# Optimization experiments

Hardware: AMD Instinct MI355X
Metric: run time of the kernel (lower is better)

The kernel has to match this reference:

```python
import jax, jax.numpy as jnp
import numpy as np

POS_W = 1.0
ANG_W = 1.0
WID_W = 1.0
N = 1048560  # predictions (divisible by 17)
M = 8388480  # total GT grasps = sum(arange(N) % 17)


def setup_inputs() -> dict:
    key = jax.random.key(0)
    k1, k2 = jax.random.split(key)
    pred = jax.random.normal(k1, (N, 6), dtype=jnp.float32)
    all_targets = jax.random.normal(k2, (M, 6), dtype=jnp.float32)
    # ragged counts in [0, 16]; sum == M exactly
    target_counts = (jnp.arange(N, dtype=jnp.int64) % 17)
    return {"pred": pred, "all_targets": all_targets, "target_counts": target_counts}


def _smooth_l1(x):
    a = jnp.abs(x)
    return jnp.where(a < 1.0, 0.5 * x * x, a - 0.5)


def reference(pred, all_targets, target_counts):
    n = pred.shape[0]
    m = all_targets.shape[0]
    # segment id for each GT row (contiguous slices, order of target_counts)
    seg = jnp.repeat(jnp.arange(n), target_counts, total_repeat_length=m)  # (M,)
    p = pred[seg]  # (M,6) gathered predictions
    dp = p[:, :2] - all_targets[:, :2]
    da = p[:, 2:4] - all_targets[:, 2:4]
    dw = p[:, 4] - all_targets[:, 4]
    dist = (POS_W * jnp.sum(dp * dp, axis=-1)
            + ANG_W * jnp.sum(da * da, axis=-1)
            + WID_W * dw * dw)  # (M,)
    # ragged argmin per segment (first occurrence, like torch.argmin)
    min_d = jax.ops.segment_min(dist, seg, num_segments=n)  # (N,)
    row = jnp.arange(m)
    cand = jnp.where(dist == min_d[seg], row, m)
    arg = jax.ops.segment_min(cand, seg, num_segments=n)  # (N,) global row idx or m
    has = target_counts > 0
    gt = all_targets[jnp.where(has, jnp.clip(arg, 0, m - 1), 0)]  # (N,6)
    # fused per-prediction loss against the closest GT
    loss_pos = jnp.sum(_smooth_l1(pred[:, :2] - gt[:, :2]), axis=-1)
    loss_ang = jnp.sum(jnp.abs(pred[:, 2:4] - gt[:, 2:4]), axis=-1)
    loss_wid = _smooth_l1(pred[:, 4] - gt[:, 4])
    losses = jnp.where(has, POS_W * loss_pos + ANG_W * loss_ang + WID_W * loss_wid, 0.0)
    return jnp.mean(losses)  # reduction='mean'
```

## Files before the change

kernel.cpp:

```cpp
#include <hip/hip_runtime.h>
#include <math.h>
#include <stdint.h>

#define POS_W 1.0f
#define ANG_W 1.0f
#define WID_W 1.0f
#define CHUNKR 2176
#define SEGMAX 52

__device__ __forceinline__ float smooth_l1(float x) {
    float a = fabsf(x);
    return a < 1.0f ? 0.5f * x * x : a - 0.5f;
}

__device__ __forceinline__ void gl_lds16(const float4* g, float4* l) {
    __builtin_amdgcn_global_load_lds(
        (const __attribute__((address_space(1))) void*)g,
        (__attribute__((address_space(3))) void*)l, 16, 0, 0);
}

__global__ void k_block_sums(const int* __restrict__ counts, int stride, int n,
                             int* __restrict__ blockSums) {
    int i = blockIdx.x * 256 + threadIdx.x;
    int c = (i < n) ? counts[(long long)i * stride] : 0;
    for (int off = 32; off > 0; off >>= 1) c += __shfl_down(c, off, 64);
    __shared__ int sdata[4];
    int lane = threadIdx.x & 63, wave = threadIdx.x >> 6;
    if (lane == 0) sdata[wave] = c;
    __syncthreads();
    if (threadIdx.x == 0)
        blockSums[blockIdx.x] = sdata[0] + sdata[1] + sdata[2] + sdata[3];
}

__global__ __launch_bounds__(256) void k_loss(
    const float* __restrict__ pred, const float* __restrict__ tgt,
    const int* __restrict__ counts, int stride, int n, int mrows,
    const int* __restrict__ blockSums, float invN, float* __restrict__ out) {
    __shared__ float4 buf[SEGMAX * 64];
    __shared__ int wsum[4];
    __shared__ int wpre[4];
    __shared__ float fs[4];

    int t = threadIdx.x;
    int lane = t & 63, wave = t >> 6;
    int b = blockIdx.x;
    int i = b * 256 + t;
    int c = (i < n) ? counts[(long long)i * stride] : 0;

    int pre = 0;
    for (int j = t; j < b; j += 256) pre += blockSums[j];

    int incl = c;
#pragma unroll
    for (int d = 1; d < 64; d <<= 1) {
        int v = __shfl_up(incl, d, 64);
        if (lane >= d) incl += v;
    }
    for (int o = 32; o > 0; o >>= 1) pre += __shfl_down(pre, o, 64);
    if (lane == 63) wsum[wave] = incl;
    if (lane == 0) wpre[wave] = pre;

    bool active = (i < n) && (c > 0);
    float p0 = 0, p1 = 0, p2 = 0, p3 = 0, p4 = 0;
    if (active) {
        const float2* p2p = (const float2*)(pred + (long long)i * 6);
        float2 a = p2p[0], bb = p2p[1], w = p2p[2];
        p0 = a.x; p1 = a.y; p2 = bb.x; p3 = bb.y; p4 = w.x;
    }
    __syncthreads();

    int w0 = wsum[0], w1 = wsum[1], w2 = wsum[2], w3 = wsum[3];
    int waveOff = (wave > 0 ? w0 : 0) + (wave > 1 ? w1 : 0) + (wave > 2 ? w2 : 0);
    int off = waveOff + incl - c;
    int total = w0 + w1 + w2 + w3;
    int winStart = wpre[0] + wpre[1] + wpre[2] + wpre[3];

    long long winB = (long long)winStart * 24;
    long long base4 = (winB & ~15ll) >> 4;
    int sh = (int)(winStart & 1);
    long long f4last = (((long long)mrows * 24) >> 4) - 1;
    const float4* tgt4 = (const float4*)tgt;
    const float2* ch2 = (const float2*)buf;

    float best = INFINITY;
    float b0 = 0, b1 = 0, b2 = 0, b3 = 0, b4 = 0;

    for (int base = 0; base < total; base += CHUNKR) {
        int rows = min(CHUNKR, total - base);
        int nF4 = (rows * 3 + sh + 1) >> 1;
        int nSeg = (nF4 + 63) >> 6;
        long long q0 = base4 + (((long long)base * 3) >> 1);
        for (int seg = wave; seg < nSeg; seg += 4) {
            long long gi = q0 + (long long)(seg << 6) + lane;
            if (gi > f4last) gi = f4last;
            gl_lds16(tgt4 + gi, &buf[seg * 64]);
        }
        asm volatile("s_waitcnt vmcnt(0)" ::: "memory");
        __builtin_amdgcn_s_barrier();
        __builtin_amdgcn_sched_barrier(0);

        if (active) {
            int lo = max(off, base), hi = min(off + c, base + rows);
            for (int rr = lo; rr < hi; ++rr) {
                int l2i = (rr - base) * 3 + sh;
                float2 ga = ch2[l2i], gb = ch2[l2i + 1], gw = ch2[l2i + 2];
                float d0 = p0 - ga.x, d1 = p1 - ga.y;
                float d2 = p2 - gb.x, d3 = p3 - gb.y;
                float d4 = p4 - gw.x;
                float dist = POS_W * (d0 * d0 + d1 * d1) +
                             ANG_W * (d2 * d2 + d3 * d3) + WID_W * d4 * d4;
                if (dist < best) {
                    best = dist;
                    b0 = ga.x; b1 = ga.y; b2 = gb.x; b3 = gb.y; b4 = gw.x;
                }
            }
        }
        if (base + CHUNKR < total) {
            asm volatile("s_waitcnt lgkmcnt(0)" ::: "memory");
            __builtin_amdgcn_s_barrier();
            __builtin_amdgcn_sched_barrier(0);
        }
    }

    float loss = 0.0f;
    if (active) {
        loss = POS_W * (smooth_l1(p0 - b0) + smooth_l1(p1 - b1)) +
               ANG_W * (fabsf(p2 - b2) + fabsf(p3 - b3)) +
               WID_W * smooth_l1(p4 - b4);
    }

    for (int o = 32; o > 0; o >>= 1) loss += __shfl_down(loss, o, 64);
    if (lane == 0) fs[wave] = loss;
    __syncthreads();
    if (t == 0) {
        float tot = (fs[0] + fs[1] + fs[2] + fs[3]) * invN;
        atomicAdd(out, tot);
    }
}

extern "C" void kernel_launch(void* const* d_in, const int* in_sizes, int n_in,
                              void* d_out, int out_size, void* d_ws,
                              size_t ws_size, hipStream_t stream) {
    const float* pred = (const float*)d_in[0];
    const float* tgt = (const float*)d_in[1];
    const int* counts = (const int*)d_in[2];
    int n = in_sizes[0] / 6;
    int mrows = in_sizes[1] / 6;
    int stride = (in_sizes[2] == n) ? 1 : 2;
    int nb = (n + 255) / 256;

    int* blockSums = (int*)d_ws;
    float* out = (float*)d_out;

    hipMemsetAsync(d_out, 0, sizeof(float), stream);
    k_block_sums<<<nb, 256, 0, stream>>>(counts, stride, n, blockSums);
    k_loss<<<nb, 256, 0, stream>>>(pred, tgt, counts, stride, n, mrows,
                                   blockSums, 1.0f / n, out);
}
```

Before: 303.0 us.

## Split target staging into two LDS halves and compute first half early

```diff
diff --git a/kernel.cpp b/kernel.cpp
--- a/kernel.cpp
+++ b/kernel.cpp
@@ -5,8 +5,11 @@
 #define POS_W 1.0f
 #define ANG_W 1.0f
 #define WID_W 1.0f
-#define CHUNKR 2176
-#define SEGMAX 52
+#define SEGS_A 28
+#define SEGS_B 24
+#define SEGS_T (SEGS_A + SEGS_B)
+#define ROWS_A 1194
+#define ROWS_PASS 2112
 
 __device__ __forceinline__ float smooth_l1(float x) {
     float a = fabsf(x);
@@ -36,7 +39,7 @@
     const float* __restrict__ pred, const float* __restrict__ tgt,
     const int* __restrict__ counts, int stride, int n, int mrows,
     const int* __restrict__ blockSums, float invN, float* __restrict__ out) {
-    __shared__ float4 buf[SEGMAX * 64];
+    __shared__ float4 buf[SEGS_T * 64];
     __shared__ int wsum[4];
     __shared__ int wpre[4];
     __shared__ float fs[4];
@@ -47,8 +50,17 @@
     int i = b * 256 + t;
     int c = (i < n) ? counts[(long long)i * stride] : 0;
 
-    int pre = 0;
-    for (int j = t; j < b; j += 256) pre += blockSums[j];
+    int pre;
+    {
+        int s0 = 0, s1 = 0, s2 = 0, s3 = 0;
+        int j = t;
+        for (; j + 768 < b; j += 1024) {
+            s0 += blockSums[j];       s1 += blockSums[j + 256];
+            s2 += blockSums[j + 512]; s3 += blockSums[j + 768];
+        }
+        for (; j < b; j += 256) s0 += blockSums[j];
+        pre = (s0 + s1) + (s2 + s3);
+    }
 
     int incl = c;
 #pragma unroll
@@ -85,40 +97,71 @@
     float best = INFINITY;
     float b0 = 0, b1 = 0, b2 = 0, b3 = 0, b4 = 0;
 
-    for (int base = 0; base < total; base += CHUNKR) {
-        int rows = min(CHUNKR, total - base);
-        int nF4 = (rows * 3 + sh + 1) >> 1;
-        int nSeg = (nF4 + 63) >> 6;
-        long long q0 = base4 + (((long long)base * 3) >> 1);
-        for (int seg = wave; seg < nSeg; seg += 4) {
-            long long gi = q0 + (long long)(seg << 6) + lane;
-            if (gi > f4last) gi = f4last;
-            gl_lds16(tgt4 + gi, &buf[seg * 64]);
-        }
-        asm volatile("s_waitcnt vmcnt(0)" ::: "memory");
-        __builtin_amdgcn_s_barrier();
-        __builtin_amdgcn_sched_barrier(0);
-
-        if (active) {
-            int lo = max(off, base), hi = min(off + c, base + rows);
-            for (int rr = lo; rr < hi; ++rr) {
-                int l2i = (rr - base) * 3 + sh;
-                float2 ga = ch2[l2i], gb = ch2[l2i + 1], gw = ch2[l2i + 2];
-                float d0 = p0 - ga.x, d1 = p1 - ga.y;
-                float d2 = p2 - gb.x, d3 = p3 - gb.y;
-                float d4 = p4 - gw.x;
-                float dist = POS_W * (d0 * d0 + d1 * d1) +
-                             ANG_W * (d2 * d2 + d3 * d3) + WID_W * d4 * d4;
-                if (dist < best) {
-                    best = dist;
-                    b0 = ga.x; b1 = ga.y; b2 = gb.x; b3 = gb.y; b4 = gw.x;
-                }
-            }
-        }
-        if (base + CHUNKR < total) {
-            asm volatile("s_waitcnt lgkmcnt(0)" ::: "memory");
+    if (total > 0) {
+        for (int base = 0; base < total; base += ROWS_PASS) {
+            int rows = min(ROWS_PASS, total - base);
+            long long q0 = base4 + (((long long)base * 3) >> 1);
+#pragma unroll
+            for (int k = 0; k < 7; ++k) {
+                int seg = wave + 4 * k;
+                long long gi = q0 + (long long)(seg << 6) + lane;
+                if (gi > f4last) gi = f4last;
+                gl_lds16(tgt4 + gi, &buf[seg * 64]);
+            }
+#pragma unroll
+            for (int k = 0; k < 6; ++k) {
+                int seg = SEGS_A + wave + 4 * k;
+                long long gi = q0 + (long long)(seg << 6) + lane;
+                if (gi > f4last) gi = f4last;
+                gl_lds16(tgt4 + gi, &buf[seg * 64]);
+            }
+            asm volatile("s_waitcnt vmcnt(6)" ::: "memory");
             __builtin_amdgcn_s_barrier();
             __builtin_amdgcn_sched_barrier(0);
+
+            int rowsA = min(rows, ROWS_A);
+            if (active) {
+                int lo = max(off, base), hi = min(off + c, base + rowsA);
+                for (int rr = lo; rr < hi; ++rr) {
+                    int l2i = (rr - base) * 3 + sh;
+                    float2 ga = ch2[l2i], gb = ch2[l2i + 1], gw = ch2[l2i + 2];
+                    float d0 = p0 - ga.x, d1 = p1 - ga.y;
+                    float d2 = p2 - gb.x, d3 = p3 - gb.y;
+                    float d4 = p4 - gw.x;
+                    float dist = POS_W * (d0 * d0 + d1 * d1) +
+                                 ANG_W * (d2 * d2 + d3 * d3) + WID_W * d4 * d4;
+                    if (dist < best) {
+                        best = dist;
+                        b0 = ga.x; b1 = ga.y; b2 = gb.x; b3 = gb.y; b4 = gw.x;
+                    }
+                }
+            }
+            asm volatile("s_waitcnt vmcnt(0)" ::: "memory");
+            __builtin_amdgcn_s_barrier();
+            __builtin_amdgcn_sched_barrier(0);
+
+            if (active && rows > ROWS_A) {
+                int lo = max(off, base + ROWS_A);
+                int hi = min(off + c, base + rows);
+                for (int rr = lo; rr < hi; ++rr) {
+                    int l2i = (rr - base) * 3 + sh;
+                    float2 ga = ch2[l2i], gb = ch2[l2i + 1], gw = ch2[l2i + 2];
+                    float d0 = p0 - ga.x, d1 = p1 - ga.y;
+                    float d2 = p2 - gb.x, d3 = p3 - gb.y;
+                    float d4 = p4 - gw.x;
+                    float dist = POS_W * (d0 * d0 + d1 * d1) +
+                                 ANG_W * (d2 * d2 + d3 * d3) + WID_W * d4 * d4;
+                    if (dist < best) {
+                        best = dist;
+                        b0 = ga.x; b1 = ga.y; b2 = gb.x; b3 = gb.y; b4 = gw.x;
+                    }
+                }
+            }
+            if (base + ROWS_PASS < total) {
+                asm volatile("s_waitcnt lgkmcnt(0)" ::: "memory");
+                __builtin_amdgcn_s_barrier();
+                __builtin_amdgcn_sched_barrier(0);
+            }
         }
     }
 
```

Result: no change. 299.7 us (-1.1%).
